# Performance work log

Hardware: AMD Instinct MI355X
Metric: run time of the kernel (lower is better)

## Reference

```python
import jax, jax.numpy as jnp
import numpy as np

B, S, C, HEADS, EXP = 8, 1024, 256, 8, 4
H = W = 32  # S = H*W
HID = EXP * C
RATES = (1, 6, 12, 18)
EPS = 1e-5


def _conv(x, w, b=None, dilation=1, padding=0):
    out = jax.lax.conv_general_dilated(
        x, w, (1, 1), [(padding, padding), (padding, padding)],
        rhs_dilation=(dilation, dilation),
        dimension_numbers=('NCHW', 'OIHW', 'NCHW'))
    if b is not None:
        out = out + b[None, :, None, None]
    return out


def _bn(x, g, b, m, v):
    # inference-mode BatchNorm2d
    s = (g / jnp.sqrt(v + EPS))[None, :, None, None]
    return (x - m[None, :, None, None]) * s + b[None, :, None, None]


def _ln(x, g, b):
    mu = jnp.mean(x, -1, keepdims=True)
    var = jnp.mean((x - mu) ** 2, -1, keepdims=True)
    return (x - mu) / jnp.sqrt(var + EPS) * g + b


def setup_inputs() -> dict:
    key = jax.random.key(0)
    ks = iter(jax.random.split(key, 64))

    def n(shape, s=0.05):
        return jax.random.normal(next(ks), shape, jnp.float32) * s

    def u(shape):
        return jax.random.uniform(next(ks), shape, jnp.float32, 0.5, 1.5)

    inp = {
        'value': n((B, S, C), 1.0),
        'key': n((B, S, C), 1.0),
        'query': n((B, S, C), 1.0),
        'res': n((B, S, C), 1.0),
        # nn.MultiheadAttention params
        'attn_wi': n((3 * C, C)), 'attn_bi': jnp.zeros((3 * C,)),
        'attn_wo': n((C, C)), 'attn_bo': jnp.zeros((C,)),
        # Modulator params
        'mod_bias': jnp.zeros((1, C, 1, 1)),
        'ca_w1': n((C // 16, C)), 'ca_w2': n((C, C // 16)),
        'pa_w': n((C, C, 1, 1)),
        'pa_bn_g': jnp.ones((C,)), 'pa_bn_b': jnp.zeros((C,)),
        'pa_bn_m': n((C,), 0.1), 'pa_bn_v': u((C,)),
        'sa_w': n((4, C, C, 3, 3)), 'sa_b': jnp.zeros((4, C)),
        'sa_bn_g': jnp.ones((4, C)), 'sa_bn_b': jnp.zeros((4, C)),
        'sa_bn_m': n((4, C), 0.1), 'sa_bn_v': u((4, C)),
        'sa_out_w': n((C, 4 * C, 1, 1)), 'sa_out_b': jnp.zeros((C,)),
        'out_w': n((C, C, 1, 1)), 'out_b': jnp.zeros((C,)),
        'out_bn_g': jnp.ones((C,)), 'out_bn_b': jnp.zeros((C,)),
        'out_bn_m': n((C,), 0.1), 'out_bn_v': u((C,)),
        # LayerNorms
        'ln1_g': jnp.ones((C,)), 'ln1_b': jnp.zeros((C,)),
        'ln2_g': jnp.ones((C,)), 'ln2_b': jnp.zeros((C,)),
        # E_MLP params
        'mlp_w1': n((HID, C)), 'mlp_b1': jnp.zeros((HID,)),
        'dw_w': n((HID, HID, 3, 3), 0.02), 'dw_b': jnp.zeros((HID,)),
        'pw_w': n((HID, HID, 3, 3), 0.02), 'pw_b': jnp.zeros((HID,)),
        'mlp_w2': n((C, HID)), 'mlp_b2': jnp.zeros((C,)),
    }
    return inp


def reference(value, key, query, res,
              attn_wi, attn_bi, attn_wo, attn_bo,
              mod_bias, ca_w1, ca_w2, pa_w,
              pa_bn_g, pa_bn_b, pa_bn_m, pa_bn_v,
              sa_w, sa_b, sa_bn_g, sa_bn_b, sa_bn_m, sa_bn_v,
              sa_out_w, sa_out_b, out_w, out_b,
              out_bn_g, out_bn_b, out_bn_m, out_bn_v,
              ln1_g, ln1_b, ln2_g, ln2_b,
              mlp_w1, mlp_b1, dw_w, dw_b, pw_w, pw_b, mlp_w2, mlp_b2):
    d = C // HEADS
    # SMA arg shuffle: block calls sma(query,key,value) -> SMA(value=query,key=key,query=value)
    # -> nn.MultiheadAttention(query=value_blk, key=key_blk, value=query_blk)
    q = (value @ attn_wi[:C].T + attn_bi[:C]).reshape(B, S, HEADS, d)
    k = (key @ attn_wi[C:2 * C].T + attn_bi[C:2 * C]).reshape(B, S, HEADS, d)
    v = (query @ attn_wi[2 * C:].T + attn_bi[2 * C:]).reshape(B, S, HEADS, d)
    scores = jnp.einsum('bqhd,bkhd->bhqk', q, k) / jnp.sqrt(jnp.float32(d))
    attn = jax.nn.softmax(scores, axis=-1)
    ctx = jnp.einsum('bhqk,bkhd->bqhd', attn, v).reshape(B, S, C)
    msa = ctx @ attn_wo.T + attn_bo                       # [B,S,C]

    x = msa.transpose(0, 2, 1).reshape(B, C, H, W)        # [B,C,H,W]

    # --- Modulator ---
    pa = x * jax.nn.sigmoid(_bn(_conv(x, pa_w), pa_bn_g, pa_bn_b, pa_bn_m, pa_bn_v))
    y = jnp.mean(x, axis=(2, 3))                          # [B,C]
    y = jax.nn.sigmoid(jax.nn.relu(y @ ca_w1.T) @ ca_w2.T)
    ca = x * y[:, :, None, None]
    pa_ca = jax.nn.softmax(pa @ ca, axis=-1)              # [B,C,H,H] (H==W)
    sa_outs = [_bn(jax.nn.relu(_conv(x, sa_w[i], sa_b[i], dilation=r, padding=r)),
                   sa_bn_g[i], sa_bn_b[i], sa_bn_m[i], sa_bn_v[i])
               for i, r in enumerate(RATES)]
    sa = _conv(jnp.concatenate(sa_outs, axis=1), sa_out_w, sa_out_b)
    out = pa_ca @ sa                                      # [B,C,H,W]
    out = _bn(_conv(out, out_w, out_b), out_bn_g, out_bn_b, out_bn_m, out_bn_v)
    syn = out + mod_bias + x                              # residual inside modulator

    attn_seq = syn.reshape(B, C, S).transpose(0, 2, 1)    # [B,S,C]
    q2 = _ln(attn_seq + res, ln1_g, ln1_b)

    # --- E_MLP ---
    h = jax.nn.gelu(q2 @ mlp_w1.T + mlp_b1, approximate=False)  # [B,S,4C]
    hc = h.transpose(0, 2, 1).reshape(B, HID, H, W)
    hc = _conv(hc, dw_w, dw_b, padding=1)
    hc = _conv(hc, pw_w, pw_b, padding=1)
    h2 = hc.reshape(B, HID, S).transpose(0, 2, 1)
    ff = h2 @ mlp_w2.T + mlp_b2
    return _ln(ff + q2, ln2_g, ln2_b)
```

## Files before the change

kernel.cpp:

```cpp
#include <hip/hip_runtime.h>
#include <hip/hip_bf16.h>
#include <math.h>

typedef __attribute__((ext_vector_type(8))) short bf16x8;
typedef __attribute__((ext_vector_type(4))) short bf16x4;
typedef __attribute__((ext_vector_type(4))) float f32x4;

#define MM 8192
#define CC 256

__device__ __forceinline__ short f2bf(float f) {
  unsigned u = __float_as_uint(f);
  u = (u + 0x7FFFu + ((u >> 16) & 1u)) >> 16;
  return (short)u;
}

__device__ __forceinline__ void gload16(const short* g, short* l) {
  __builtin_amdgcn_global_load_lds(
      (const __attribute__((address_space(1))) unsigned int*)(g),
      (__attribute__((address_space(3))) unsigned int*)(l), 16, 0, 0);
}

__global__ __launch_bounds__(256, 2) void convh_k(const short* __restrict__ Ain,
                                                  const short* __restrict__ Wt,
                                                  short* __restrict__ outB,
                                                  const float* __restrict__ bias) {
  extern __shared__ short sm[];
  const int tid = threadIdx.x;
  const int bx = blockIdx.x;
  const int bm = bx >> 3, bn = bx & 7;
  const int l = tid & 63, w = tid >> 6;
  const int wm = w >> 1, wn = w & 1;
  const int lr = l & 15, lg = l >> 4;
  const int lsub = l >> 3;
  const int srcu = (l & 7) ^ lsub;
  const int img = bm >> 3, rbase = (bm & 7) * 4;
  const bf16x8 zv = {0, 0, 0, 0, 0, 0, 0, 0};

  f32x4 acc[4][4];
#pragma unroll
  for (int i = 0; i < 4; ++i)
#pragma unroll
    for (int j = 0; j < 4; ++j) acc[i][j] = (f32x4){0.f, 0.f, 0.f, 0.f};

  const short* wsrc[4];
#pragma unroll
  for (int i = 0; i < 4; ++i) {
    int rowi = (w * 4 + i) * 8 + lsub;
    wsrc[i] = Wt + (size_t)(bn * 128 + rowi) * 1024 + srcu * 8;
  }

  const short* asrc[6]; int apos[6]; bool avalid[6];
#pragma unroll
  for (int i = 0; i < 6; ++i) {
    int ug = tid + i * 256;
    int pos = ug >> 3, u = ug & 7;
    int irow = pos >> 5, px = pos & 31;
    int grow = rbase + irow - 1;
    avalid[i] = ((unsigned)grow < 32u);
    int growc = grow < 0 ? 0 : (grow > 31 ? 31 : grow);
    asrc[i] = Ain + ((size_t)(img * 1024 + growc * 32 + px)) * 1024 + u * 8;
    apos[i] = pos * 64 + ((u ^ (pos & 7)) << 3);
  }

  bf16x8 areg[6];
  auto issueA = [&](int kc) {
#pragma unroll
    for (int i = 0; i < 6; ++i)
      areg[i] = *(const bf16x8*)(asrc[i] + kc * 64);
  };
  auto writeA = [&](int ab) {
    short* abuf = sm + 16384 + ab * 12288;
#pragma unroll
    for (int i = 0; i < 6; ++i)
      *(bf16x8*)(abuf + apos[i]) = avalid[i] ? areg[i] : zv;
  };
  auto issueW = [&](int kc, int tap, int wb) {
    short* base = sm + wb * 8192;
    size_t wo = (size_t)tap * 1048576 + (size_t)kc * 64;
#pragma unroll
    for (int i = 0; i < 4; ++i)
      gload16(wsrc[i] + wo, base + (w * 4 + i) * 512);
  };
  auto compute = [&](int dy, int dx, const short* bA, const short* bB) {
    __builtin_amdgcn_s_setprio(1);
#pragma unroll
    for (int ks = 0; ks < 64; ks += 32) {
      const int u = (ks >> 3) + lg;
      bf16x8 af[4], bfr[4];
#pragma unroll
      for (int mt = 0; mt < 4; ++mt) {
        int px = (mt & 1) * 16 + lr;
        int ipx = px + dx;
        bool okx = ((unsigned)ipx < 32u);
        int pos = (wm * 2 + (mt >> 1) + 1 + dy) * 32 + (ipx & 31);
        bf16x8 v = *(const bf16x8*)&bA[pos * 64 + ((u ^ (pos & 7)) << 3)];
        af[mt] = okx ? v : zv;
      }
#pragma unroll
      for (int nt = 0; nt < 4; ++nt)
        bfr[nt] = *(const bf16x8*)&bB[(wn * 64 + nt * 16 + lr) * 64 + ((u ^ (lr & 7)) << 3)];
#pragma unroll
      for (int mt = 0; mt < 4; ++mt)
#pragma unroll
        for (int nt = 0; nt < 4; ++nt)
          acc[mt][nt] = __builtin_amdgcn_mfma_f32_16x16x32_bf16(af[mt], bfr[nt], acc[mt][nt], 0, 0, 0);
    }
    __builtin_amdgcn_s_setprio(0);
  };

  issueA(0);
  issueW(0, 0, 0);
  issueW(0, 1, 1);
  asm volatile("s_waitcnt vmcnt(4)" ::: "memory");
  writeA(0);
  asm volatile("s_waitcnt lgkmcnt(0)" ::: "memory");

  for (int kc = 0; kc < 16; ++kc) {
    const int ab = kc & 1;
    const short* bA = sm + 16384 + ab * 12288;
#pragma unroll
    for (int tap = 0; tap < 9; ++tap) {
      const int wb = (kc + tap) & 1;
      const short* bB = sm + wb * 8192;
      if (tap == 7) {
        if (kc < 15) asm volatile("s_waitcnt vmcnt(10)" ::: "memory");
        else         asm volatile("s_waitcnt vmcnt(4)" ::: "memory");
      } else if (tap == 8) {
        if (kc < 15) asm volatile("s_waitcnt vmcnt(4)" ::: "memory");
        else         asm volatile("s_waitcnt vmcnt(0)" ::: "memory");
      } else {
        asm volatile("s_waitcnt vmcnt(4)" ::: "memory");
      }
      asm volatile("s_barrier" ::: "memory");
      compute(tap / 3 - 1, tap % 3 - 1, bA, bB);
      asm volatile("s_barrier" ::: "memory");
      if (tap <= 6) {
        if (tap == 6 && kc < 15) issueA(kc + 1);
        issueW(kc, tap + 2, wb);
      } else if (tap == 7) {
        if (kc < 15) issueW(kc + 1, 0, wb);
      } else {
        if (kc < 15) {
          writeA(ab ^ 1);
          asm volatile("s_waitcnt lgkmcnt(0)" ::: "memory");
          issueW(kc + 1, 1, wb);
        }
      }
    }
  }

#pragma unroll
  for (int nt = 0; nt < 4; ++nt) {
    const int col = bn * 128 + wn * 64 + nt * 16 + lr;
    const float bi = bias[col];
#pragma unroll
    for (int mt = 0; mt < 4; ++mt) {
      const int row0 = bm * 128 + wm * 64 + mt * 16 + lg * 4;
#pragma unroll
      for (int j = 0; j < 4; ++j)
        outB[(size_t)(row0 + j) * 1024 + col] = f2bf(acc[mt][nt][j] + bi);
    }
  }
}

struct GP {
  const short* A; const short* W; float* outF; short* outB; float* outT;
  const float* bias; const float* scale; const float* shift; const float* aux;
  const short* zero;
  long aZStride, wZStride, oZStride;
  int N, Kc, ldA, ldOut, outColOff, outZOff;
  int dil0, dil1, dil2, dil3;
  int T, nkcs;
};

template<int TAPS, int EPI, int OUTMODE, int TSTORE, int HALF>
__global__ __launch_bounds__(256, 2) void gemmd_k(GP p) {
  extern __shared__ short sm[];
  constexpr int RG   = HALF ? 2 : 4;
  constexpr int MT   = HALF ? 2 : 4;
  constexpr int NT   = HALF ? 2 : 4;
  constexpr int WTs  = HALF ? 32 : 64;
  constexpr int BMr  = HALF ? 64 : 128;
  constexpr int BNr  = HALF ? 64 : 128;
  constexpr int BSTR = HALF ? 8192 : 16384;
  constexpr int BOFF = HALF ? 4096 : 8192;
  const int tid = threadIdx.x;
  const int bx = blockIdx.x, bz = blockIdx.z;
  const int bm = HALF ? (bx >> 2) : (bx & 63);
  const int bn = HALF ? (bx & 3) : (bx >> 6);
  const int l = tid & 63, w = tid >> 6;
  const int wm = w >> 1, wn = w & 1;
  const int lr = l & 15, lg = l >> 4;
  const int lsub = l >> 3;
  const int srcu = (l & 7) ^ lsub;

  const short* Abase = p.A + (size_t)bz * p.aZStride;
  const short* Wbase = p.W + (size_t)bz * p.wZStride;
  const int dil = (TAPS == 9)
      ? (bz == 0 ? p.dil0 : bz == 1 ? p.dil1 : bz == 2 ? p.dil2 : p.dil3) : 1;

  f32x4 acc[MT][NT];
#pragma unroll
  for (int i = 0; i < MT; ++i)
#pragma unroll
    for (int j = 0; j < NT; ++j) acc[i][j] = (f32x4){0.f, 0.f, 0.f, 0.f};

  int rowi[RG], prow[RG], bimg[RG], py[RG], px[RG];
  const short* wsrc[RG];
#pragma unroll
  for (int i = 0; i < RG; ++i) {
    rowi[i] = (w * RG + i) * 8 + lsub;
    prow[i] = bm * BMr + rowi[i];
    bimg[i] = prow[i] >> 10; py[i] = (prow[i] >> 5) & 31; px[i] = prow[i] & 31;
    wsrc[i] = Wbase + (size_t)(bn * BNr + rowi[i]) * p.Kc + srcu * 8;
  }
  const size_t wTap = (size_t)p.N * p.Kc;
  const int nkcMask = (1 << p.nkcs) - 1;

  auto issue = [&](int t, int buf) {
    const int tap = t >> p.nkcs;
    const int kc = t & nkcMask;
    short* base = sm + buf * BSTR;
    if (TAPS == 1) {
#pragma unroll
      for (int i = 0; i < RG; ++i)
        gload16(Abase + (size_t)prow[i] * p.ldA + kc * 64 + srcu * 8,
                base + (w * RG + i) * 512);
    } else {
      const int dy = (tap / 3 - 1) * dil, dx = (tap % 3 - 1) * dil;
#pragma unroll
      for (int i = 0; i < RG; ++i) {
        int yy = py[i] + dy, xx = px[i] + dx;
        bool ok = ((unsigned)yy < 32u) & ((unsigned)xx < 32u);
        const short* a = ok
            ? Abase + (size_t)((bimg[i] << 10) + (yy << 5) + xx) * p.ldA + kc * 64
            : p.zero;
        gload16(a + srcu * 8, base + (w * RG + i) * 512);
      }
    }
    short* bbase = base + BOFF;
    const size_t wo = (size_t)tap * wTap + kc * 64;
#pragma unroll
    for (int i = 0; i < RG; ++i)
      gload16(wsrc[i] + wo, bbase + (w * RG + i) * 512);
  };

  auto compute = [&](int buf) {
    const short* bA = sm + buf * BSTR;
    const short* bB = bA + BOFF;
    __builtin_amdgcn_s_setprio(1);
#pragma unroll
    for (int ks = 0; ks < 64; ks += 32) {
      const int u = (ks >> 3) + lg;
      bf16x8 af[MT], bfr[NT];
#pragma unroll
      for (int mt = 0; mt < MT; ++mt)
        af[mt] = *(bf16x8*)&bA[(wm * WTs + mt * 16 + lr) * 64 + ((u ^ (lr & 7)) << 3)];
#pragma unroll
      for (int nt = 0; nt < NT; ++nt)
        bfr[nt] = *(bf16x8*)&bB[(wn * WTs + nt * 16 + lr) * 64 + ((u ^ (lr & 7)) << 3)];
#pragma unroll
      for (int mt = 0; mt < MT; ++mt)
#pragma unroll
        for (int nt = 0; nt < NT; ++nt)
          acc[mt][nt] = __builtin_amdgcn_mfma_f32_16x16x32_bf16(af[mt], bfr[nt], acc[mt][nt], 0, 0, 0);
    }
    __builtin_amdgcn_s_setprio(0);
  };

  issue(0, 0);
  if (p.T > 1) issue(1, 1);
  int cur = 0;
  for (int t = 0; t < p.T; ++t) {
    if (t + 1 < p.T) {
      if (HALF) asm volatile("s_waitcnt vmcnt(4)" ::: "memory");
      else      asm volatile("s_waitcnt vmcnt(8)" ::: "memory");
    } else {
      asm volatile("s_waitcnt vmcnt(0)" ::: "memory");
    }
    asm volatile("s_barrier" ::: "memory");
    compute(cur);
    asm volatile("s_barrier" ::: "memory");
    if (t + 2 < p.T) issue(t + 2, cur);
    cur ^= 1;
  }

  float* outF = p.outF + (size_t)bz * p.oZStride;
  short* outB = p.outB + (size_t)bz * p.oZStride;
#pragma unroll
  for (int nt = 0; nt < NT; ++nt) {
    const int col = bn * BNr + wn * WTs + nt * 16 + lr;
    const int gcol = p.outColOff + bz * p.outZOff + col;
    const float bi = (p.bias != nullptr) ? p.bias[bz * p.N + col] : 0.f;
    float scl = 0.f, shf = 0.f;
    if (EPI == 3 || EPI == 4 || EPI == 5) {
      scl = p.scale[bz * p.N + col]; shf = p.shift[bz * p.N + col];
    }
#pragma unroll
    for (int mt = 0; mt < MT; ++mt) {
      const int row0 = bm * BMr + wm * WTs + mt * 16 + lg * 4;
      f32x4 vv;
#pragma unroll
      for (int j = 0; j < 4; ++j) {
        const long row = row0 + j;
        float v = acc[mt][nt][j];
        if (EPI == 1 || EPI == 2 || EPI == 3) v += bi;
        if (EPI == 2) v = 0.5f * v * (1.f + erff(v * 0.70710678118654752f));
        if (EPI == 3) { v = fmaxf(v, 0.f); v = v * scl + shf; }
        if (EPI == 4) {
          float t2 = v * scl + shf;
          float sg = 1.f / (1.f + __expf(-t2));
          v = p.aux[row * 256 + col] * sg;
        }
        if (EPI == 5) v = v * scl + shf + p.aux[row * 256 + col];
        vv[j] = v;
        if (OUTMODE == 0 || OUTMODE == 2) outF[row * (long)p.ldOut + gcol] = v;
        if (OUTMODE == 1 || OUTMODE == 2) outB[row * (long)p.ldOut + gcol] = f2bf(v);
      }
      if (TSTORE) {
        float* t = p.outT + ((size_t)(row0 >> 10) * 256 + gcol) * 1024 + (row0 & 1023);
        *(f32x4*)t = vv;
      }
    }
  }
}

__global__ __launch_bounds__(256) void attn_k(const short* qb, const short* kb,
                                              const short* vb, short* ctx) {
  __shared__ short lK[128 * 40];
  __shared__ short lVt[32 * 136];
  __shared__ short lP[4][16 * 136];
  const int tid = threadIdx.x;
  const int qt = blockIdx.x;
  const int bh = blockIdx.y;
  const int b = bh >> 3, h = bh & 7;
  const int l = tid & 63, wv = tid >> 6;
  const int lr = l & 15, lg = l >> 4;
  const float SC = 0.17677669529663687f;

  const int qrow = qt * 64 + wv * 16 + lr;
  const bf16x8 qf = *(const bf16x8*)(qb + ((size_t)(b * 1024 + qrow)) * 256 + h * 32 + lg * 8);

  f32x4 o0 = {0.f,0.f,0.f,0.f}, o1 = {0.f,0.f,0.f,0.f};
  float m[4] = {-1e30f, -1e30f, -1e30f, -1e30f};
  float lsum[4] = {0.f, 0.f, 0.f, 0.f};

  for (int ch = 0; ch < 8; ++ch) {
    __syncthreads();
    {
      const int keyi = tid >> 1, d0 = (tid & 1) * 16;
      const short* src = kb + ((size_t)(b * 1024 + ch * 128 + keyi)) * 256 + h * 32 + d0;
      short* dst = &lK[keyi * 40 + d0];
      *(bf16x8*)dst = *(const bf16x8*)src;
      *(bf16x8*)(dst + 8) = *(const bf16x8*)(src + 8);
    }
    {
      const int keyi = tid >> 1, d0 = (tid & 1) * 16;
      const short* src = vb + ((size_t)(b * 1024 + ch * 128 + keyi)) * 256 + h * 32 + d0;
      short tmp[16];
      *(bf16x8*)tmp = *(const bf16x8*)src;
      *(bf16x8*)(tmp + 8) = *(const bf16x8*)(src + 8);
#pragma unroll
      for (int j = 0; j < 16; ++j) lVt[(d0 + j) * 136 + keyi] = tmp[j];
    }
    __syncthreads();

    f32x4 sc[8];
#pragma unroll
    for (int jt = 0; jt < 8; ++jt) {
      bf16x8 bfr = *(bf16x8*)&lK[(jt * 16 + lr) * 40 + lg * 8];
      sc[jt] = __builtin_amdgcn_mfma_f32_16x16x32_bf16(qf, bfr, (f32x4){0.f,0.f,0.f,0.f}, 0, 0, 0);
      sc[jt] *= SC;
    }
#pragma unroll
    for (int j = 0; j < 4; ++j) {
      float rm = -1e30f;
#pragma unroll
      for (int jt = 0; jt < 8; ++jt) rm = fmaxf(rm, sc[jt][j]);
      rm = fmaxf(rm, __shfl_xor(rm, 1));
      rm = fmaxf(rm, __shfl_xor(rm, 2));
      rm = fmaxf(rm, __shfl_xor(rm, 4));
      rm = fmaxf(rm, __shfl_xor(rm, 8));
      float mn = fmaxf(m[j], rm);
      float alpha = exp2f((m[j] - mn) * 1.44269504088896f);
      m[j] = mn;
      float rs = 0.f;
#pragma unroll
      for (int jt = 0; jt < 8; ++jt) {
        float pv = exp2f((sc[jt][j] - mn) * 1.44269504088896f);
        sc[jt][j] = pv;
        rs += pv;
      }
      rs += __shfl_xor(rs, 1); rs += __shfl_xor(rs, 2);
      rs += __shfl_xor(rs, 4); rs += __shfl_xor(rs, 8);
      lsum[j] = lsum[j] * alpha + rs;
      o0[j] *= alpha; o1[j] *= alpha;
      const int prw = lg * 4 + j;
#pragma unroll
      for (int jt = 0; jt < 8; ++jt) lP[wv][prw * 136 + jt * 16 + lr] = f2bf(sc[jt][j]);
    }
#pragma unroll
    for (int kc = 0; kc < 4; ++kc) {
      bf16x8 pf = *(bf16x8*)&lP[wv][lr * 136 + kc * 32 + lg * 8];
      bf16x8 v0 = *(bf16x8*)&lVt[lr * 136 + kc * 32 + lg * 8];
      bf16x8 v1 = *(bf16x8*)&lVt[(16 + lr) * 136 + kc * 32 + lg * 8];
      o0 = __builtin_amdgcn_mfma_f32_16x16x32_bf16(pf, v0, o0, 0, 0, 0);
      o1 = __builtin_amdgcn_mfma_f32_16x16x32_bf16(pf, v1, o1, 0, 0, 0);
    }
  }
  const size_t orow = (size_t)(b * 1024 + qt * 64 + wv * 16);
#pragma unroll
  for (int j = 0; j < 4; ++j) {
    float inv = 1.f / lsum[j];
    ctx[(orow + lg * 4 + j) * 256 + h * 32 + lr]      = f2bf(o0[j] * inv);
    ctx[(orow + lg * 4 + j) * 256 + h * 32 + 16 + lr] = f2bf(o1[j] * inv);
  }
}

__global__ __launch_bounds__(256) void cvt4_k(const float* src, short* dst, int n4) {
  int i = blockIdx.x * 256 + threadIdx.x;
  if (i < n4) {
    f32x4 v = ((const f32x4*)src)[i];
    bf16x4 o;
    o[0] = f2bf(v[0]); o[1] = f2bf(v[1]); o[2] = f2bf(v[2]); o[3] = f2bf(v[3]);
    ((bf16x4*)dst)[i] = o;
  }
}

__global__ __launch_bounds__(256) void zero_k(short* p) {
  p[blockIdx.x * 256 + threadIdx.x] = 0;
}

__global__ __launch_bounds__(256) void tap_k(const float* src, short* dst, int n) {
  int i = blockIdx.x * 256 + threadIdx.x;
  if (i >= n) return;
  const float* s = src + (size_t)i * 9;
  float v[9];
#pragma unroll
  for (int t = 0; t < 9; ++t) v[t] = s[t];
#pragma unroll
  for (int t = 0; t < 9; ++t) dst[(size_t)t * n + i] = f2bf(v[t]);
}

__global__ void bnprep_k(const float* pg, const float* pb, const float* pm, const float* pv,
                         const float* sg, const float* sb, const float* sm, const float* sv,
                         const float* og, const float* ob, const float* om, const float* ov,
                         const float* conv_ob, const float* mbias, float* out) {
  int c = threadIdx.x;
  float s = pg[c] / sqrtf(pv[c] + 1e-5f);
  out[c] = s;
  out[256 + c] = pb[c] - pm[c] * s;
  for (int i = 0; i < 4; ++i) {
    int idx = i * 256 + c;
    float ss = sg[idx] / sqrtf(sv[idx] + 1e-5f);
    out[512 + idx] = ss;
    out[1536 + idx] = sb[idx] - sm[idx] * ss;
  }
  float os = og[c] / sqrtf(ov[c] + 1e-5f);
  out[2560 + c] = os;
  out[2816 + c] = ob[c] - om[c] * os + conv_ob[c] * os + mbias[c];
}

__global__ __launch_bounds__(256) void tposeb_k(const float* src, short* dst) {
  __shared__ float tile[32][33];
  int pc = blockIdx.x, cc = blockIdx.y, b = blockIdx.z;
  int tx = threadIdx.x & 31, ty = threadIdx.x >> 5;
  const float* s = src + ((size_t)b * 256 + cc * 32) * 1024 + pc * 32;
#pragma unroll
  for (int k = 0; k < 4; ++k)
    tile[ty + 8 * k][tx] = s[(ty + 8 * k) * 1024 + tx];
  __syncthreads();
  short* d = dst + ((size_t)b * 1024 + pc * 32) * 256 + cc * 32;
#pragma unroll
  for (int k = 0; k < 4; ++k)
    d[(ty + 8 * k) * 256 + tx] = f2bf(tile[tx][ty + 8 * k]);
}

__global__ __launch_bounds__(256) void camean_k(const float* x, float* partial) {
  int blk = blockIdx.x, c = threadIdx.x;
  const float* px = x + ((size_t)blk * 64) * 256 + c;
  float s = 0.f;
#pragma unroll 4
  for (int r = 0; r < 64; ++r) s += px[(size_t)r * 256];
  partial[blk * 256 + c] = s;
}

__global__ __launch_bounds__(256) void ca2_k(const float* partial, const float* w1,
                                             const float* w2, float* y2) {
  __shared__ float ly[256];
  __shared__ float ly1[16];
  int b = blockIdx.x, c = threadIdx.x;
  float s = 0.f;
#pragma unroll
  for (int j = 0; j < 16; ++j) s += partial[(b * 16 + j) * 256 + c];
  ly[c] = s * (1.f / 1024.f);
  __syncthreads();
  if (c < 16) {
    float a = 0.f;
    const float* wp = w1 + c * 256;
    for (int i = 0; i < 256; ++i) a += ly[i] * wp[i];
    ly1[c] = fmaxf(a, 0.f);
  }
  __syncthreads();
  float a = 0.f;
  const float* wp = w2 + c * 16;
#pragma unroll
  for (int j = 0; j < 16; ++j) a += ly1[j] * wp[j];
  y2[b * 256 + c] = 1.f / (1.f + __expf(-a));
}

__global__ __launch_bounds__(256) void bm1_k(const float* paT, const float* xT,
                                             const float* y2, float* pa_ca) {
  __shared__ float sp[32][33], sx[32][33], so[32][33];
  __shared__ float rinv[32];
  int bc = blockIdx.x, t = threadIdx.x;
  for (int e = t; e < 1024; e += 256) {
    sp[e >> 5][e & 31] = paT[(size_t)bc * 1024 + e];
    sx[e >> 5][e & 31] = xT[(size_t)bc * 1024 + e];
  }
  __syncthreads();
  float yv = y2[bc];
  int i = t >> 3, j0 = (t & 7) * 4;
  float a0 = 0.f, a1 = 0.f, a2 = 0.f, a3 = 0.f;
  for (int k = 0; k < 32; ++k) {
    float pv = sp[i][k];
    a0 += pv * sx[k][j0];     a1 += pv * sx[k][j0 + 1];
    a2 += pv * sx[k][j0 + 2]; a3 += pv * sx[k][j0 + 3];
  }
  so[i][j0] = a0 * yv; so[i][j0 + 1] = a1 * yv;
  so[i][j0 + 2] = a2 * yv; so[i][j0 + 3] = a3 * yv;
  __syncthreads();
  if (t < 32) {
    float mx = -1e30f;
    for (int j = 0; j < 32; ++j) mx = fmaxf(mx, so[t][j]);
    float sum = 0.f;
    for (int j = 0; j < 32; ++j) { float pp = __expf(so[t][j] - mx); so[t][j] = pp; sum += pp; }
    rinv[t] = 1.f / sum;
  }
  __syncthreads();
  for (int e = t; e < 1024; e += 256)
    pa_ca[(size_t)bc * 1024 + e] = so[e >> 5][e & 31] * rinv[e >> 5];
}

__global__ __launch_bounds__(256) void bm2_k(const float* pa_ca, const float* saT, float* moT) {
  __shared__ float sp[32][33], ss[32][33];
  int bc = blockIdx.x, t = threadIdx.x;
  for (int e = t; e < 1024; e += 256) {
    sp[e >> 5][e & 31] = pa_ca[(size_t)bc * 1024 + e];
    ss[e >> 5][e & 31] = saT[(size_t)bc * 1024 + e];
  }
  __syncthreads();
  int i = t >> 3, j0 = (t & 7) * 4;
  float a0 = 0.f, a1 = 0.f, a2 = 0.f, a3 = 0.f;
  for (int k = 0; k < 32; ++k) {
    float pv = sp[i][k];
    a0 += pv * ss[k][j0];     a1 += pv * ss[k][j0 + 1];
    a2 += pv * ss[k][j0 + 2]; a3 += pv * ss[k][j0 + 3];
  }
  size_t base = (size_t)bc * 1024 + i * 32 + j0;
  moT[base] = a0; moT[base + 1] = a1; moT[base + 2] = a2; moT[base + 3] = a3;
}

template<int DUAL>
__global__ __launch_bounds__(256) void ln_k(const float* in, const float* res,
                                            const float* g, const float* bta,
                                            float* out, short* outB) {
  __shared__ float red[8];
  size_t row = blockIdx.x;
  int c = threadIdx.x;
  int wv = c >> 6, lane = c & 63;
  float v = in[row * 256 + c] + res[row * 256 + c];
  float s = v;
  for (int mk = 1; mk < 64; mk <<= 1) s += __shfl_xor(s, mk);
  if (lane == 0) red[wv] = s;
  __syncthreads();
  float mu = (red[0] + red[1] + red[2] + red[3]) * (1.f / 256.f);
  float d = v - mu;
  float q = d * d;
  for (int mk = 1; mk < 64; mk <<= 1) q += __shfl_xor(q, mk);
  if (lane == 0) red[4 + wv] = q;
  __syncthreads();
  float var = (red[4] + red[5] + red[6] + red[7]) * (1.f / 256.f);
  float o = d * rsqrtf(var + 1e-5f) * g[c] + bta[c];
  out[row * 256 + c] = o;
  if (DUAL) outB[row * 256 + c] = f2bf(o);
}

extern "C" void kernel_launch(void* const* d_in, const int* in_sizes, int n_in,
                              void* d_out, int out_size, void* d_ws, size_t ws_size,
                              hipStream_t stream) {
  (void)in_sizes; (void)n_in; (void)out_size; (void)ws_size;
  const float* value    = (const float*)d_in[0];
  const float* key      = (const float*)d_in[1];
  const float* query    = (const float*)d_in[2];
  const float* res      = (const float*)d_in[3];
  const float* attn_wi  = (const float*)d_in[4];
  const float* attn_bi  = (const float*)d_in[5];
  const float* attn_wo  = (const float*)d_in[6];
  const float* attn_bo  = (const float*)d_in[7];
  const float* mod_bias = (const float*)d_in[8];
  const float* ca_w1    = (const float*)d_in[9];
  const float* ca_w2    = (const float*)d_in[10];
  const float* pa_w     = (const float*)d_in[11];
  const float* pa_bn_g  = (const float*)d_in[12];
  const float* pa_bn_b  = (const float*)d_in[13];
  const float* pa_bn_m  = (const float*)d_in[14];
  const float* pa_bn_v  = (const float*)d_in[15];
  const float* sa_w     = (const float*)d_in[16];
  const float* sa_b     = (const float*)d_in[17];
  const float* sa_bn_g  = (const float*)d_in[18];
  const float* sa_bn_b  = (const float*)d_in[19];
  const float* sa_bn_m  = (const float*)d_in[20];
  const float* sa_bn_v  = (const float*)d_in[21];
  const float* sa_out_w = (const float*)d_in[22];
  const float* sa_out_b = (const float*)d_in[23];
  const float* out_w    = (const float*)d_in[24];
  const float* out_b    = (const float*)d_in[25];
  const float* out_bn_g = (const float*)d_in[26];
  const float* out_bn_b = (const float*)d_in[27];
  const float* out_bn_m = (const float*)d_in[28];
  const float* out_bn_v = (const float*)d_in[29];
  const float* ln1_g    = (const float*)d_in[30];
  const float* ln1_b    = (const float*)d_in[31];
  const float* ln2_g    = (const float*)d_in[32];
  const float* ln2_b    = (const float*)d_in[33];
  const float* mlp_w1   = (const float*)d_in[34];
  const float* mlp_b1   = (const float*)d_in[35];
  const float* dw_w     = (const float*)d_in[36];
  const float* dw_b     = (const float*)d_in[37];
  const float* pw_w     = (const float*)d_in[38];
  const float* pw_b     = (const float*)d_in[39];
  const float* mlp_w2   = (const float*)d_in[40];
  const float* mlp_b2   = (const float*)d_in[41];

  char* ws = (char*)d_ws;
  const size_t MB = 1024 * 1024;
  char* A = ws + 0 * MB;
  char* Bx = ws + 16 * MB;
  char* Cx = ws + 32 * MB;
  float* xbuf  = (float*)(ws + 40 * MB);
  short* xbf   = (short*)(ws + 48 * MB);
  char* Fx = ws + 52 * MB;
  float* q2buf = (float*)(ws + 60 * MB);
  short* q2B   = (short*)(ws + 68 * MB);
  short* wdw   = (short*)(ws + 72 * MB);
  short* wpw   = (short*)(ws + 90 * MB);
  size_t o = 108 * MB;
  short* w_awi  = (short*)(ws + o); o += 768 * 256 * 2;
  short* w_awo  = (short*)(ws + o); o += 256 * 256 * 2;
  short* w_pa   = (short*)(ws + o); o += 256 * 256 * 2;
  short* w_sa   = (short*)(ws + o); o += (size_t)4 * 9 * 256 * 256 * 2;
  short* w_saou = (short*)(ws + o); o += 256 * 1024 * 2;
  short* w_out  = (short*)(ws + o); o += 256 * 256 * 2;
  short* w_mlp1 = (short*)(ws + o); o += 1024 * 256 * 2;
  short* w_mlp2 = (short*)(ws + o); o += 256 * 1024 * 2;
  float* bn     = (float*)(ws + o); o += 3072 * 4;
  float* y2buf  = (float*)(ws + o); o += 8 * 256 * 4;
  float* capart = (float*)(ws + o); o += 128 * 256 * 4;
  short* zbuf   = (short*)(ws + o); o += 2048 * 2;

  short* vkq  = (short*)A;
  short* qkv  = (short*)Bx;
  short* ctxB = (short*)Cx;
  float* xT   = (float*)A;
  float* paT  = (float*)(A + 8 * MB);
  float* pa_ca = (float*)Bx;
  short* saCat = (short*)A;
  float* saT  = (float*)Cx;
  float* moT  = (float*)Fx;
  short* modB = (short*)Cx;
  float* synBuf = (float*)Fx;
  short* hB   = (short*)A;
  short* hc1B = (short*)Bx;
  short* h2B  = (short*)A;
  float* ffBuf = (float*)Cx;

  const int LDSB = 2 * 16384 * 2;
  const int LDSH = 2 * 8192 * 2;
  const int LDSC = 40960 * 2;
  hipFuncSetAttribute((const void*)gemmd_k<1, 1, 1, 0, 1>, hipFuncAttributeMaxDynamicSharedMemorySize, LDSH);
  hipFuncSetAttribute((const void*)gemmd_k<1, 1, 2, 1, 1>, hipFuncAttributeMaxDynamicSharedMemorySize, LDSH);
  hipFuncSetAttribute((const void*)gemmd_k<1, 4, 3, 1, 1>, hipFuncAttributeMaxDynamicSharedMemorySize, LDSH);
  hipFuncSetAttribute((const void*)gemmd_k<9, 3, 1, 0, 0>, hipFuncAttributeMaxDynamicSharedMemorySize, LDSB);
  hipFuncSetAttribute((const void*)gemmd_k<1, 1, 3, 1, 1>, hipFuncAttributeMaxDynamicSharedMemorySize, LDSH);
  hipFuncSetAttribute((const void*)gemmd_k<1, 5, 0, 0, 1>, hipFuncAttributeMaxDynamicSharedMemorySize, LDSH);
  hipFuncSetAttribute((const void*)gemmd_k<1, 2, 1, 0, 0>, hipFuncAttributeMaxDynamicSharedMemorySize, LDSB);
  hipFuncSetAttribute((const void*)gemmd_k<1, 1, 0, 0, 1>, hipFuncAttributeMaxDynamicSharedMemorySize, LDSH);
  hipFuncSetAttribute((const void*)convh_k, hipFuncAttributeMaxDynamicSharedMemorySize, LDSC);

  zero_k<<<8, 256, 0, stream>>>(zbuf);
  cvt4_k<<<192, 256, 0, stream>>>(attn_wi, w_awi, 768 * 64);
  cvt4_k<<<64, 256, 0, stream>>>(attn_wo, w_awo, 256 * 64);
  cvt4_k<<<64, 256, 0, stream>>>(pa_w, w_pa, 256 * 64);
  for (int i4 = 0; i4 < 4; ++i4)
    tap_k<<<256, 256, 0, stream>>>(sa_w + (size_t)i4 * 589824,
                                   w_sa + (size_t)i4 * 589824, 65536);
  cvt4_k<<<256, 256, 0, stream>>>(sa_out_w, w_saou, 1024 * 64);
  cvt4_k<<<64, 256, 0, stream>>>(out_w, w_out, 256 * 64);
  cvt4_k<<<256, 256, 0, stream>>>(mlp_w1, w_mlp1, 1024 * 64);
  cvt4_k<<<256, 256, 0, stream>>>(mlp_w2, w_mlp2, 1024 * 64);
  tap_k<<<4096, 256, 0, stream>>>(dw_w, wdw, 1048576);
  tap_k<<<4096, 256, 0, stream>>>(pw_w, wpw, 1048576);
  bnprep_k<<<1, 256, 0, stream>>>(pa_bn_g, pa_bn_b, pa_bn_m, pa_bn_v,
                                  sa_bn_g, sa_bn_b, sa_bn_m, sa_bn_v,
                                  out_bn_g, out_bn_b, out_bn_m, out_bn_v,
                                  out_b, mod_bias, bn);
  cvt4_k<<<2048, 256, 0, stream>>>(value, vkq, MM * 64);
  cvt4_k<<<2048, 256, 0, stream>>>(key,   vkq + (size_t)MM * 256, MM * 64);
  cvt4_k<<<2048, 256, 0, stream>>>(query, vkq + (size_t)2 * MM * 256, MM * 64);

  GP g;
  g.zero = zbuf; g.scale = nullptr; g.shift = nullptr; g.aux = nullptr;
  g.aZStride = 0; g.wZStride = 0; g.oZStride = 0;
  g.outColOff = 0; g.outZOff = 0;
  g.dil0 = 1; g.dil1 = 1; g.dil2 = 1; g.dil3 = 1;
  g.outF = nullptr; g.outB = nullptr; g.outT = nullptr;

  g.A = vkq; g.W = w_awi; g.outB = qkv; g.bias = attn_bi;
  g.N = 256; g.Kc = 256; g.ldA = 256; g.ldOut = 256; g.T = 4; g.nkcs = 2;
  g.aZStride = (size_t)MM * 256; g.wZStride = 256 * 256; g.oZStride = (size_t)MM * 256;
  gemmd_k<1, 1, 1, 0, 1><<<dim3(512, 1, 3), 256, LDSH, stream>>>(g);
  g.aZStride = 0; g.wZStride = 0; g.oZStride = 0;

  attn_k<<<dim3(16, 64), 256, 0, stream>>>(qkv, qkv + (size_t)MM * 256,
                                           qkv + (size_t)2 * MM * 256, ctxB);

  g.A = ctxB; g.W = w_awo; g.outF = xbuf; g.outB = xbf; g.outT = xT; g.bias = attn_bo;
  gemmd_k<1, 1, 2, 1, 1><<<dim3(512), 256, LDSH, stream>>>(g);

  g.A = xbf; g.W = w_pa; g.outF = nullptr; g.outB = nullptr; g.outT = paT; g.bias = nullptr;
  g.scale = bn; g.shift = bn + 256; g.aux = xbuf;
  gemmd_k<1, 4, 3, 1, 1><<<dim3(512), 256, LDSH, stream>>>(g);
  g.scale = nullptr; g.shift = nullptr; g.aux = nullptr;

  camean_k<<<128, 256, 0, stream>>>(xbuf, capart);
  ca2_k<<<8, 256, 0, stream>>>(capart, ca_w1, ca_w2, y2buf);
  bm1_k<<<2048, 256, 0, stream>>>(paT, xT, y2buf, pa_ca);

  g.A = xbf; g.W = w_sa; g.outB = saCat; g.outF = nullptr; g.outT = nullptr;
  g.bias = sa_b; g.scale = bn + 512; g.shift = bn + 1536;
  g.ldOut = 1024; g.outZOff = 256; g.wZStride = (size_t)9 * 256 * 256;
  g.dil0 = 1; g.dil1 = 6; g.dil2 = 12; g.dil3 = 18;
  g.T = 36; g.nkcs = 2;
  gemmd_k<9, 3, 1, 0, 0><<<dim3(128, 1, 4), 256, LDSB, stream>>>(g);
  g.outZOff = 0; g.wZStride = 0; g.scale = nullptr; g.shift = nullptr;
  g.dil0 = 1; g.dil1 = 1; g.dil2 = 1; g.dil3 = 1;

  g.A = saCat; g.W = w_saou; g.outB = nullptr; g.outT = saT; g.bias = sa_out_b;
  g.N = 256; g.Kc = 1024; g.ldA = 1024; g.ldOut = 256; g.T = 16; g.nkcs = 4;
  gemmd_k<1, 1, 3, 1, 1><<<dim3(512), 256, LDSH, stream>>>(g);

  bm2_k<<<2048, 256, 0, stream>>>(pa_ca, saT, moT);
  tposeb_k<<<dim3(32, 8, 8), 256, 0, stream>>>(moT, modB);

  g.A = modB; g.W = w_out; g.outF = synBuf; g.outT = nullptr; g.bias = nullptr;
  g.scale = bn + 2560; g.shift = bn + 2816; g.aux = xbuf;
  g.N = 256; g.Kc = 256; g.ldA = 256; g.ldOut = 256; g.T = 4; g.nkcs = 2;
  gemmd_k<1, 5, 0, 0, 1><<<dim3(512), 256, LDSH, stream>>>(g);
  g.scale = nullptr; g.shift = nullptr; g.aux = nullptr;

  ln_k<1><<<8192, 256, 0, stream>>>(synBuf, res, ln1_g, ln1_b, q2buf, q2B);

  g.A = q2B; g.W = w_mlp1; g.outB = hB; g.outF = nullptr; g.bias = mlp_b1;
  g.N = 1024; g.Kc = 256; g.ldA = 256; g.ldOut = 1024; g.T = 4; g.nkcs = 2;
  gemmd_k<1, 2, 1, 0, 0><<<dim3(512), 256, LDSB, stream>>>(g);

  convh_k<<<dim3(512), 256, LDSC, stream>>>(hB, wdw, hc1B, dw_b);

  convh_k<<<dim3(512), 256, LDSC, stream>>>(hc1B, wpw, h2B, pw_b);

  g.A = h2B; g.W = w_mlp2; g.outF = ffBuf; g.outB = nullptr; g.bias = mlp_b2;
  g.N = 256; g.Kc = 1024; g.ldA = 1024; g.ldOut = 256; g.T = 16; g.nkcs = 4;
  gemmd_k<1, 1, 0, 0, 1><<<dim3(512), 256, LDSH, stream>>>(g);

  ln_k<0><<<8192, 256, 0, stream>>>(ffBuf, q2buf, ln2_g, ln2_b, (float*)d_out, nullptr);
}
```

Measured before the change: 540.9 us.

## Restructure 3x3 conv pipeline to triple-buffered weights and single A buffer

The implicit-GEMM 3x3 conv kernel switches from double-buffered A and W tiles to a single A tile plus three rotating W tap buffers. The tap loop is hand-unrolled with prefetch two taps ahead, and the kc loop is kept rolled. The next A chunk is loaded into registers during the taps and written to LDS only after the final barrier. LDS use drops from 80KB to 72KB, but the A write is now serialised at the end of each kc iteration, adding a stall.

```diff
diff --git a/kernel.cpp b/kernel.cpp
--- a/kernel.cpp
+++ b/kernel.cpp
@@ -36,6 +36,7 @@
   const int srcu = (l & 7) ^ lsub;
   const int img = bm >> 3, rbase = (bm & 7) * 4;
   const bf16x8 zv = {0, 0, 0, 0, 0, 0, 0, 0};
+  short* const aBuf = sm + 24576;
 
   f32x4 acc[4][4];
 #pragma unroll
@@ -69,20 +70,19 @@
     for (int i = 0; i < 6; ++i)
       areg[i] = *(const bf16x8*)(asrc[i] + kc * 64);
   };
-  auto writeA = [&](int ab) {
-    short* abuf = sm + 16384 + ab * 12288;
+  auto writeA = [&]() {
 #pragma unroll
     for (int i = 0; i < 6; ++i)
-      *(bf16x8*)(abuf + apos[i]) = avalid[i] ? areg[i] : zv;
+      *(bf16x8*)(aBuf + apos[i]) = avalid[i] ? areg[i] : zv;
   };
-  auto issueW = [&](int kc, int tap, int wb) {
-    short* base = sm + wb * 8192;
+  auto issueW = [&](int kc, int tap, int wOff) {
+    short* base = sm + wOff;
     size_t wo = (size_t)tap * 1048576 + (size_t)kc * 64;
 #pragma unroll
     for (int i = 0; i < 4; ++i)
       gload16(wsrc[i] + wo, base + (w * 4 + i) * 512);
   };
-  auto compute = [&](int dy, int dx, const short* bA, const short* bB) {
+  auto compute = [&](int dy, int dx, const short* bB) {
     __builtin_amdgcn_s_setprio(1);
 #pragma unroll
     for (int ks = 0; ks < 64; ks += 32) {
@@ -94,7 +94,7 @@
         int ipx = px + dx;
         bool okx = ((unsigned)ipx < 32u);
         int pos = (wm * 2 + (mt >> 1) + 1 + dy) * 32 + (ipx & 31);
-        bf16x8 v = *(const bf16x8*)&bA[pos * 64 + ((u ^ (pos & 7)) << 3)];
+        bf16x8 v = *(const bf16x8*)&aBuf[pos * 64 + ((u ^ (pos & 7)) << 3)];
         af[mt] = okx ? v : zv;
       }
 #pragma unroll
@@ -109,46 +109,56 @@
     __builtin_amdgcn_s_setprio(0);
   };
 
+#define VM(n)  asm volatile("s_waitcnt vmcnt(" #n ")" ::: "memory")
+#define BAR()  asm volatile("s_barrier" ::: "memory")
+
   issueA(0);
+  VM(0);
+  writeA();
   issueW(0, 0, 0);
-  issueW(0, 1, 1);
-  asm volatile("s_waitcnt vmcnt(4)" ::: "memory");
-  writeA(0);
+  issueW(0, 1, 8192);
   asm volatile("s_waitcnt lgkmcnt(0)" ::: "memory");
 
+#pragma unroll 1
   for (int kc = 0; kc < 16; ++kc) {
-    const int ab = kc & 1;
-    const short* bA = sm + 16384 + ab * 12288;
-#pragma unroll
-    for (int tap = 0; tap < 9; ++tap) {
-      const int wb = (kc + tap) & 1;
-      const short* bB = sm + wb * 8192;
-      if (tap == 7) {
-        if (kc < 15) asm volatile("s_waitcnt vmcnt(10)" ::: "memory");
-        else         asm volatile("s_waitcnt vmcnt(4)" ::: "memory");
-      } else if (tap == 8) {
-        if (kc < 15) asm volatile("s_waitcnt vmcnt(4)" ::: "memory");
-        else         asm volatile("s_waitcnt vmcnt(0)" ::: "memory");
-      } else {
-        asm volatile("s_waitcnt vmcnt(4)" ::: "memory");
-      }
-      asm volatile("s_barrier" ::: "memory");
-      compute(tap / 3 - 1, tap % 3 - 1, bA, bB);
-      asm volatile("s_barrier" ::: "memory");
-      if (tap <= 6) {
-        if (tap == 6 && kc < 15) issueA(kc + 1);
-        issueW(kc, tap + 2, wb);
-      } else if (tap == 7) {
-        if (kc < 15) issueW(kc + 1, 0, wb);
-      } else {
-        if (kc < 15) {
-          writeA(ab ^ 1);
-          asm volatile("s_waitcnt lgkmcnt(0)" ::: "memory");
-          issueW(kc + 1, 1, wb);
-        }
-      }
-    }
-  }
+    VM(4); BAR();
+    compute(-1, -1, sm);
+    if (kc < 15) issueA(kc + 1);
+    issueW(kc, 2, 16384);
+    if (kc < 15) { VM(10); } else { VM(4); }
+    BAR();
+    compute(-1, 0, sm + 8192);
+    issueW(kc, 3, 0);
+    VM(4); BAR();
+    compute(-1, 1, sm + 16384);
+    issueW(kc, 4, 8192);
+    VM(4); BAR();
+    compute(0, -1, sm);
+    issueW(kc, 5, 16384);
+    VM(4); BAR();
+    compute(0, 0, sm + 8192);
+    issueW(kc, 6, 0);
+    VM(4); BAR();
+    compute(0, 1, sm + 16384);
+    issueW(kc, 7, 8192);
+    VM(4); BAR();
+    compute(1, -1, sm);
+    issueW(kc, 8, 16384);
+    VM(4); BAR();
+    compute(1, 0, sm + 8192);
+    if (kc < 15) issueW(kc + 1, 0, 0);
+    if (kc < 15) { VM(4); } else { VM(0); }
+    BAR();
+    compute(1, 1, sm + 16384);
+    if (kc < 15) issueW(kc + 1, 1, 8192);
+    BAR();
+    if (kc < 15) {
+      writeA();
+      asm volatile("s_waitcnt lgkmcnt(0)" ::: "memory");
+    }
+  }
+#undef VM
+#undef BAR
 
 #pragma unroll
   for (int nt = 0; nt < 4; ++nt) {
@@ -678,7 +688,7 @@
 
   const int LDSB = 2 * 16384 * 2;
   const int LDSH = 2 * 8192 * 2;
-  const int LDSC = 40960 * 2;
+  const int LDSC = 36864 * 2;
   hipFuncSetAttribute((const void*)gemmd_k<1, 1, 1, 0, 1>, hipFuncAttributeMaxDynamicSharedMemorySize, LDSH);
   hipFuncSetAttribute((const void*)gemmd_k<1, 1, 2, 1, 1>, hipFuncAttributeMaxDynamicSharedMemorySize, LDSH);
   hipFuncSetAttribute((const void*)gemmd_k<1, 4, 3, 1, 1>, hipFuncAttributeMaxDynamicSharedMemorySize, LDSH);
```

Result: no change. 551.2 us (+1.9%).
